# Performance work log

Hardware: AMD Instinct MI355X
Metric: run time of the kernel (lower is better)

The kernel has to match this reference:

```python
import jax, jax.numpy as jnp
import numpy as np

B, C, Ci, H, W = 4, 256, 128, 64, 64  # batch, in_channels, inter_channels, spatial
BN_EPS = 1e-5


def setup_inputs() -> dict:
    key = jax.random.key(0)
    ks = jax.random.split(key, 8)
    s = (2.0 / C) ** 0.5  # kaiming fan_in std for 1x1 conv over C inputs
    return {
        "a": jax.random.normal(ks[0], (B, C, H, W), jnp.float32),
        "b": jax.random.normal(ks[1], (B, C, H, W), jnp.float32),
        "theta_w": jax.random.normal(ks[2], (Ci, C), jnp.float32) * s,
        "theta_b": jnp.zeros((Ci,), jnp.float32),
        "phi_w": jax.random.normal(ks[3], (Ci, C), jnp.float32) * s,
        "phi_b": jnp.zeros((Ci,), jnp.float32),
        "g_w": jax.random.normal(ks[4], (Ci, C), jnp.float32) * s,
        "g_b": jnp.zeros((Ci,), jnp.float32),
        "W_w": jax.random.normal(ks[5], (C, Ci), jnp.float32) * (2.0 / Ci) ** 0.5,
        "bn_gamma": jnp.ones((C,), jnp.float32),
        "bn_beta": jnp.zeros((C,), jnp.float32),
        "bn_mean": jnp.zeros((C,), jnp.float32),
        "bn_var": jnp.ones((C,), jnp.float32),
    }


def _conv1x1(x, w, bias=None):
    # x: [B,Cin,H,W], w: [Cout,Cin] -> [B,Cout,H,W]
    y = jnp.einsum("oc,bchw->bohw", w, x)
    if bias is not None:
        y = y + bias[None, :, None, None]
    return y


def reference(a, b, theta_w, theta_b, phi_w, phi_b, g_w, g_b, W_w,
              bn_gamma, bn_beta, bn_mean, bn_var):
    Bsz, _, h, w = a.shape
    n = h * w
    theta_a = _conv1x1(a, theta_w, theta_b).reshape(Bsz, Ci, n).transpose(0, 2, 1)  # [B,N,Ci]
    phi_b_ = _conv1x1(b, phi_w, phi_b).reshape(Bsz, Ci, n)                          # [B,Ci,N]
    f = jnp.einsum("bnc,bcm->bnm", theta_a, phi_b_) / n                             # [B,N,N]
    g_b_ = _conv1x1(b, g_w, g_b).reshape(Bsz, Ci, n).transpose(0, 2, 1)             # [B,N,Ci]
    y = jnp.einsum("bnm,bmc->bnc", f, g_b_)                                         # [B,N,Ci]
    y = y.transpose(0, 2, 1).reshape(Bsz, Ci, h, w)
    wy = _conv1x1(y, W_w)                                                           # no bias
    inv = jax.lax.rsqrt(bn_var + BN_EPS)
    out = (wy - bn_mean[None, :, None, None]) * (bn_gamma * inv)[None, :, None, None] \
          + bn_beta[None, :, None, None]
    return out
```

## Files before the change

### kernel.cpp

```cpp
#include <hip/hip_runtime.h>
#include <hip/hip_bf16.h>

#define NSP 4096
#define CCH 256
#define CIN 128
#define BN_EPS 1e-5f

typedef __bf16 bf16x8 __attribute__((ext_vector_type(8)));
typedef __bf16 bf16x4 __attribute__((ext_vector_type(4)));
typedef float f32x4 __attribute__((ext_vector_type(4)));
typedef unsigned short u16x8 __attribute__((ext_vector_type(8)));

typedef const __attribute__((address_space(1))) unsigned int gu32;
typedef __attribute__((address_space(3))) unsigned int lu32;

__constant__ int IT10[10] = {0,0,0,0,1,1,1,2,2,3};
__constant__ int JT10[10] = {0,1,2,3,1,2,3,2,3,3};


__device__ __forceinline__ float4 fetch_tr(const float* __restrict__ A, int lda, int m0,
                                           int k0, int tid) {
  const int r = tid >> 2, kq = (tid & 3) << 2;
  return *(const float4*)(A + (size_t)(m0 + r) * lda + k0 + kq);
}
__device__ __forceinline__ void stash_tr(float (*As)[68], float4 v, int tid) {
  const int r = tid >> 2, kq = (tid & 3) << 2;
  As[kq + 0][r] = v.x; As[kq + 1][r] = v.y; As[kq + 2][r] = v.z; As[kq + 3][r] = v.w;
}
__device__ __forceinline__ float4 fetch_dir(const float* __restrict__ B, int ldb, int k0,
                                            int n0, int tid) {
  const int kr = tid >> 4, nq = (tid & 15) << 2;
  return *(const float4*)(B + (size_t)(k0 + kr) * ldb + n0 + nq);
}
__device__ __forceinline__ void stash_dir(float (*Bs)[68], float4 v, int tid) {
  const int kr = tid >> 4, nq = (tid & 15) << 2;
  *(float4*)(&Bs[kr][nq]) = v;
}

__device__ __forceinline__ void mm16(const float (*As)[68], const float (*Bs)[68],
                                     float acc[4][4], int ty, int tx) {
#pragma unroll
  for (int kk = 0; kk < 16; ++kk) {
    const float4 av = *(const float4*)(&As[kk][ty << 2]);
    const float4 bv = *(const float4*)(&Bs[kk][tx << 2]);
    const float ar[4] = {av.x, av.y, av.z, av.w};
    const float br[4] = {bv.x, bv.y, bv.z, bv.w};
#pragma unroll
    for (int i = 0; i < 4; ++i)
#pragma unroll
      for (int j = 0; j < 4; ++j) acc[i][j] += ar[i] * br[j];
  }
}

__device__ __forceinline__ float wave_reduce(float v) {
#pragma unroll
  for (int off = 32; off; off >>= 1) v += __shfl_down(v, off);
  return v;
}

__global__ __launch_bounds__(256) void prep_kernel(
    const float* __restrict__ bin, const float* __restrict__ a,
    const float* __restrict__ W_w, const float* __restrict__ g_w,
    const float* __restrict__ phi_w, const float* __restrict__ theta_w,
    const float* __restrict__ phi_b, const float* __restrict__ theta_b,
    const float* __restrict__ g_b,
    __bf16* __restrict__ bhi, __bf16* __restrict__ blo,
    float* __restrict__ srow,
    float* __restrict__ Wg, __bf16* __restrict__ Wghi, __bf16* __restrict__ Wglo,
    __bf16* __restrict__ PTthi, __bf16* __restrict__ PTtlo,
    __bf16* __restrict__ at,
    float* __restrict__ vb_g, float* __restrict__ vpt, float* __restrict__ wgb,
    float* __restrict__ dvec) {
  __shared__ float smem[64 * 68];
  const int idx = blockIdx.x;
  const int t = threadIdx.x;
  const int wave = t >> 6, lane = t & 63;
  if (idx < 1024) {
    const int row = idx;
    const float* src = bin + (size_t)row * NSP + t * 16;
    float sum = 0.f;
    unsigned short h16[16], l16[16];
#pragma unroll
    for (int i = 0; i < 4; ++i) {
      const float4 v = *(const float4*)(src + i * 4);
      const float vv[4] = {v.x, v.y, v.z, v.w};
      sum += v.x + v.y + v.z + v.w;
#pragma unroll
      for (int e = 0; e < 4; ++e) {
        const unsigned u = __float_as_uint(vv[e]);
        h16[i * 4 + e] = (unsigned short)(u >> 16);
        const float hf = __uint_as_float(u & 0xffff0000u);
        l16[i * 4 + e] = (unsigned short)(__float_as_uint(vv[e] - hf) >> 16);
      }
    }
    unsigned short* dh = (unsigned short*)bhi + (size_t)row * NSP + t * 16;
    unsigned short* dl = (unsigned short*)blo + (size_t)row * NSP + t * 16;
    *(u16x8*)dh = *(u16x8*)&h16[0];
    *(u16x8*)(dh + 8) = *(u16x8*)&h16[8];
    *(u16x8*)dl = *(u16x8*)&l16[0];
    *(u16x8*)(dl + 8) = *(u16x8*)&l16[8];
#pragma unroll
    for (int off = 32; off; off >>= 1) sum += __shfl_down(sum, off);
    if (lane == 0) smem[wave] = sum;
    __syncthreads();
    if (t == 0) srow[row] = smem[0] + smem[1] + smem[2] + smem[3];
  } else if (idx < 2048) {
    const int p = idx - 1024;
    const int n0 = (p & 63) * 64, c0 = ((p >> 6) & 3) * 64, b = p >> 8;
    float (*tile)[68] = (float(*)[68])smem;
    const int cr = t >> 4, nq = (t & 15) << 2;
    const float* src = a + ((size_t)(b * CCH + c0)) * NSP + n0;
#pragma unroll
    for (int s = 0; s < 4; ++s) {
      const float4 v = *(const float4*)(src + (size_t)(cr + s * 16) * NSP + nq);
      *(float4*)&tile[cr + s * 16][nq] = v;
    }
    __syncthreads();
    const int n = t >> 2, cq = (t & 3) << 4;
    __bf16 outv[16];
#pragma unroll
    for (int i = 0; i < 16; ++i) outv[i] = (__bf16)tile[cq + i][n];
    __bf16* dst = at + ((size_t)(b * NSP + n0 + n)) * CCH + c0 + cq;
    *(bf16x8*)dst = *(bf16x8*)&outv[0];
    *(bf16x8*)(dst + 8) = *(bf16x8*)&outv[8];
  } else if (idx < 2080) {
    const int p = idx - 2048;
    const int zsel = p >> 4, rem = p & 15;
    const int m0 = (rem >> 2) * 64, n0 = (rem & 3) * 64;
    float (*As)[68] = (float(*)[68])smem;
    float (*Bs)[68] = (float(*)[68])(smem + 16 * 68);
    const int ty = t >> 4, tx = t & 15;
    float acc[4][4] = {};
    if (zsel == 0) {
      float4 ar = fetch_tr(W_w, CIN, m0, 0, t);
      float4 br = fetch_dir(g_w, CCH, 0, n0, t);
      for (int kt = 0; kt < 8; ++kt) {
        stash_tr(As, ar, t); stash_dir(Bs, br, t);
        __syncthreads();
        if (kt < 7) { ar = fetch_tr(W_w, CIN, m0, (kt + 1) * 16, t);
                      br = fetch_dir(g_w, CCH, (kt + 1) * 16, n0, t); }
        mm16(As, Bs, acc, ty, tx);
        __syncthreads();
      }
#pragma unroll
      for (int i = 0; i < 4; ++i) {
        const size_t off = (size_t)(m0 + (ty << 2) + i) * 256 + n0 + (tx << 2);
        *(float4*)(Wg + off) = make_float4(acc[i][0], acc[i][1], acc[i][2], acc[i][3]);
        __bf16 h4[4], l4[4];
#pragma unroll
        for (int j = 0; j < 4; ++j) {
          const __bf16 h = (__bf16)acc[i][j];
          h4[j] = h; l4[j] = (__bf16)(acc[i][j] - (float)h);
        }
        *(bf16x4*)(Wghi + off) = *(bf16x4*)h4;
        *(bf16x4*)(Wglo + off) = *(bf16x4*)l4;
      }
    } else {
      float4 ar = fetch_dir(theta_w, CCH, 0, m0, t);
      float4 br = fetch_dir(phi_w, CCH, 0, n0, t);
      for (int kt = 0; kt < 8; ++kt) {
        stash_dir(As, ar, t); stash_dir(Bs, br, t);
        __syncthreads();
        if (kt < 7) { ar = fetch_dir(theta_w, CCH, (kt + 1) * 16, m0, t);
                      br = fetch_dir(phi_w, CCH, (kt + 1) * 16, n0, t); }
        mm16(As, Bs, acc, ty, tx);
        __syncthreads();
      }
#pragma unroll
      for (int i = 0; i < 4; ++i) {
        const size_t off = (size_t)(m0 + (ty << 2) + i) * 256 + n0 + (tx << 2);
        __bf16 h4[4], l4[4];
#pragma unroll
        for (int j = 0; j < 4; ++j) {
          const __bf16 h = (__bf16)acc[i][j];
          h4[j] = h; l4[j] = (__bf16)(acc[i][j] - (float)h);
        }
        *(bf16x4*)(PTthi + off) = *(bf16x4*)h4;
        *(bf16x4*)(PTtlo + off) = *(bf16x4*)l4;
      }
    }
  } else if (idx == 2080) {
    float* tb_s = smem;
    float* pb_s = smem + 128;
    if (t < 128) { tb_s[t] = theta_b[t]; pb_s[t] = phi_b[t]; }
    __syncthreads();
    float acc = 0.f;
#pragma unroll 8
    for (int i = 0; i < 128; ++i) acc += phi_w[(size_t)i * 256 + t] * tb_s[i];
    vb_g[t] = acc;
    if (t < 64) {
      float pv = pb_s[t] * tb_s[t] + pb_s[t + 64] * tb_s[t + 64];
      pv = wave_reduce(pv);
      if (t == 0) dvec[0] = pv;
    }
  } else if (idx == 2081) {
    float* pb_s = smem;
    if (t < 128) pb_s[t] = phi_b[t];
    __syncthreads();
    float acc = 0.f;
#pragma unroll 8
    for (int i = 0; i < 128; ++i) acc += pb_s[i] * theta_w[(size_t)i * 256 + t];
    vpt[t] = acc;
  } else {
    const int p = idx - 2082;
    float* gb_s = smem;
    if (t < 128) gb_s[t] = g_b[t];
    __syncthreads();
    const float2 gv = *(const float2*)&gb_s[lane * 2];
    for (int i = 0; i < 16; ++i) {
      const int o = p * 64 + wave * 16 + i;
      const float2 r = *(const float2*)(W_w + (size_t)o * 128 + lane * 2);
      float v = fmaf(r.x, gv.x, r.y * gv.y);
      v = wave_reduce(v);
      if (lane == 0) wgb[o] = v;
    }
  }
}

__global__ __launch_bounds__(256) void gram_kernel(
    const __bf16* __restrict__ bhi, const __bf16* __restrict__ blo,
    float* __restrict__ Gpart,
    const float* __restrict__ srow, const float* __restrict__ Wg,
    const __bf16* __restrict__ PTthi, const __bf16* __restrict__ PTtlo,
    const float* __restrict__ vb_g,
    float* __restrict__ Wgs, float* __restrict__ sPTv, float* __restrict__ dvec) {
  __shared__ __align__(16) __bf16 AtBt[2][2][64][64];
  auto& At = AtBt[0];
  auto& Bt = AtBt[1];
  const int idx = blockIdx.x;
  const int t = threadIdx.x;
  const int wave = t >> 6, lane = t & 63;
  if (idx < 320) {
    const int kc = idx & 7;
    const int rest = idx >> 3;
    const int tile = rest % 10;
    const int batch = rest / 10;
    const int it = IT10[tile], jt = JT10[tile];
    const bool diag = (it == jt);
    const int m = lane & 15, q = lane >> 4;
    const size_t rowbase = (size_t)batch * CCH;
    const int colbase = kc * 512;
    const int rseg = lane >> 3, ch = lane & 7;
    const int u = ch ^ rseg;
    const int h = u >> 2, j = u & 3;
    const __bf16* gsrc = h ? blo : bhi;

    auto stage = [&](int ph, int ks) {
#pragma unroll
      for (int c = 0; c < 4; ++c) {
        const int s = wave * 4 + c;
        const int isB = s >> 3;
        if (diag && isB) continue;
        const int kb = s & 7;
        const int grow = (isB ? jt : it) * 64 + kb * 8 + rseg;
        const __bf16* gp = gsrc + (rowbase + (size_t)grow) * NSP +
                           colbase + ks * 32 + j * 8;
        const __bf16* lp = isB ? &Bt[ph][kb * 8][0] : &At[ph][kb * 8][0];
        __builtin_amdgcn_global_load_lds((gu32*)(const void*)gp,
                                         (lu32*)(void*)lp, 16, 0, 0);
      }
    };

    f32x4 acc[4] = {};
    const int chA = q ^ (m & 7);
    stage(0, 0);
    int ph = 0;
    for (int ks = 0; ks < 16; ++ks) {
      __syncthreads();
      if (ks < 15) stage(ph ^ 1, ks + 1);
      const bf16x8 ah = *(const bf16x8*)&At[ph][wave * 16 + m][chA * 8];
      const bf16x8 al = *(const bf16x8*)&At[ph][wave * 16 + m][(chA ^ 4) * 8];
      const __bf16 (*Bsrc)[64] = diag ? At[ph] : Bt[ph];
#pragma unroll
      for (int t4 = 0; t4 < 4; ++t4) {
        const bf16x8 bh = *(const bf16x8*)&Bsrc[t4 * 16 + m][chA * 8];
        const bf16x8 bl = *(const bf16x8*)&Bsrc[t4 * 16 + m][(chA ^ 4) * 8];
        acc[t4] = __builtin_amdgcn_mfma_f32_16x16x32_bf16(ah, bh, acc[t4], 0, 0, 0);
        acc[t4] = __builtin_amdgcn_mfma_f32_16x16x32_bf16(ah, bl, acc[t4], 0, 0, 0);
        acc[t4] = __builtin_amdgcn_mfma_f32_16x16x32_bf16(al, bh, acc[t4], 0, 0, 0);
      }
      ph ^= 1;
    }
    float* Gp = Gpart + ((size_t)(kc * 4 + batch)) * 65536;
#pragma unroll
    for (int t4 = 0; t4 < 4; ++t4)
#pragma unroll
      for (int r = 0; r < 4; ++r)
        Gp[(size_t)(it * 64 + wave * 16 + q * 4 + r) * 256 + jt * 64 + t4 * 16 + m] =
            acc[t4][r];
    if (!diag) {
      __syncthreads();
      float* Tf = (float*)AtBt;
#pragma unroll
      for (int t4 = 0; t4 < 4; ++t4)
#pragma unroll
        for (int r = 0; r < 4; ++r)
          Tf[(t4 * 16 + m) * 68 + wave * 16 + q * 4 + r] = acc[t4][r];
      __syncthreads();
      const int rr = t >> 2, cq = (t & 3) * 16;
      float* Gpt = Gp + (size_t)(jt * 64 + rr) * 256 + it * 64 + cq;
#pragma unroll
      for (int i = 0; i < 4; ++i)
        *(float4*)(Gpt + i * 4) = *(const float4*)&Tf[rr * 68 + cq + i * 4];
    }
  } else {
    float* lds = (float*)AtBt;
    const int p = idx - 320;
    const int b = p >> 4, seg = p & 15;
    lds[t] = srow[b * 256 + t];
    __syncthreads();
    const float4 sv = *(const float4*)&lds[lane * 4];
    for (int i = wave; i < 16; i += 4) {
      const int o = seg * 16 + i;
      const float4 r = *(const float4*)(Wg + (size_t)o * 256 + lane * 4);
      float v = fmaf(r.x, sv.x, fmaf(r.y, sv.y, fmaf(r.z, sv.z, r.w * sv.w)));
      v = wave_reduce(v);
      if (lane == 0) Wgs[b * 256 + o] = v;
    }
    for (int i = wave; i < 16; i += 4) {
      const int c = seg * 16 + i;
      const bf16x4 ph = *(const bf16x4*)(PTthi + (size_t)c * 256 + lane * 4);
      const bf16x4 pl = *(const bf16x4*)(PTtlo + (size_t)c * 256 + lane * 4);
      const float svv[4] = {sv.x, sv.y, sv.z, sv.w};
      float v = 0.f;
#pragma unroll
      for (int e = 0; e < 4; ++e) v += ((float)ph[e] + (float)pl[e]) * svv[e];
      v = wave_reduce(v);
      if (lane == 0) sPTv[b * 256 + c] = v;
    }
    if (seg == 0 && wave == 0) {
      const float4 vbv = *(const float4*)(vb_g + lane * 4);
      float v = fmaf(vbv.x, sv.x, fmaf(vbv.y, sv.y, fmaf(vbv.z, sv.z, vbv.w * sv.w)));
      v = wave_reduce(v);
      if (lane == 0) dvec[1 + b] = v;
    }
  }
}

__global__ __launch_bounds__(256) void redw2_kernel(
    const float* __restrict__ Gpart, const float* __restrict__ vb_g,
    float* __restrict__ t2_g,
    const __bf16* __restrict__ Wghi, const __bf16* __restrict__ Wglo,
    __bf16* __restrict__ W2hi, __bf16* __restrict__ W2lo) {
  const int blk = blockIdx.x;
  const int t = threadIdx.x;
  const int wave = t >> 6, lane = t & 63;
  __shared__ __bf16 Gsh[16][264], Gsl[16][264];
  const int b = blk >> 4, nt = blk & 15;
  const int rr = t >> 4;
  const int c0 = (t & 15) * 16;
  f32x4 s[4] = {};
#pragma unroll
  for (int p = 0; p < 8; ++p) {
    const float* src = Gpart + (((size_t)(p * 4 + b)) << 16) +
                       (size_t)(nt * 16 + rr) * 256 + c0;
#pragma unroll
    for (int e = 0; e < 4; ++e) s[e] += *(const f32x4*)(src + e * 4);
  }
  {
    float part = 0.f;
#pragma unroll
    for (int e = 0; e < 4; ++e) {
      const float4 vv = *(const float4*)(vb_g + c0 + e * 4);
      part += s[e][0] * vv.x + s[e][1] * vv.y + s[e][2] * vv.z + s[e][3] * vv.w;
    }
#pragma unroll
    for (int off = 8; off; off >>= 1) part += __shfl_down(part, off);
    if ((t & 15) == 0) t2_g[b * 256 + nt * 16 + rr] = part;
  }
  __bf16 h8[16], l8[16];
#pragma unroll
  for (int e = 0; e < 16; ++e) {
    const float x = s[e >> 2][e & 3];
    const __bf16 h = (__bf16)x;
    h8[e] = h; l8[e] = (__bf16)(x - (float)h);
  }
  *(bf16x8*)&Gsh[rr][c0] = *(bf16x8*)&h8[0];
  *(bf16x8*)&Gsh[rr][c0 + 8] = *(bf16x8*)&h8[8];
  *(bf16x8*)&Gsl[rr][c0] = *(bf16x8*)&l8[0];
  *(bf16x8*)&Gsl[rr][c0 + 8] = *(bf16x8*)&l8[8];
  __syncthreads();
  const int m = lane & 15, q = lane >> 4;
  f32x4 acc[4] = {};
#pragma unroll
  for (int ks = 0; ks < 8; ++ks) {
    const int k = ks * 32 + q * 8;
    const bf16x8 bh = *(const bf16x8*)&Gsh[m][k];
    const bf16x8 bl = *(const bf16x8*)&Gsl[m][k];
#pragma unroll
    for (int i = 0; i < 4; ++i) {
      const int mt = i * 4 + wave;
      const bf16x8 ah = *(const bf16x8*)(Wghi + (size_t)(mt * 16 + m) * 256 + k);
      const bf16x8 al = *(const bf16x8*)(Wglo + (size_t)(mt * 16 + m) * 256 + k);
      acc[i] = __builtin_amdgcn_mfma_f32_16x16x32_bf16(ah, bh, acc[i], 0, 0, 0);
      acc[i] = __builtin_amdgcn_mfma_f32_16x16x32_bf16(ah, bl, acc[i], 0, 0, 0);
      acc[i] = __builtin_amdgcn_mfma_f32_16x16x32_bf16(al, bh, acc[i], 0, 0, 0);
    }
  }
#pragma unroll
  for (int i = 0; i < 4; ++i) {
    const int mt = i * 4 + wave;
#pragma unroll
    for (int r = 0; r < 4; ++r) {
      const size_t off = ((size_t)b << 16) + (size_t)(mt * 16 + q * 4 + r) * 256 +
                         nt * 16 + m;
      const float v = acc[i][r];
      const __bf16 h = (__bf16)v;
      W2hi[off] = h;
      W2lo[off] = (__bf16)(v - (float)h);
    }
  }
}

__global__ __launch_bounds__(256) void wout_mfma_kernel(
    const __bf16* __restrict__ W2hi, const __bf16* __restrict__ W2lo,
    const __bf16* __restrict__ PTthi, const __bf16* __restrict__ PTtlo,
    const float* __restrict__ Wgs, const float* __restrict__ sPT,
    const float* __restrict__ wgb, const float* __restrict__ vpt,
    const float* __restrict__ Wg, const float* __restrict__ t2_g,
    const float* __restrict__ dvec,
    const float* __restrict__ bn_gamma, const float* __restrict__ bn_beta,
    const float* __restrict__ bn_mean, const float* __restrict__ bn_var,
    __bf16* __restrict__ Whi, __bf16* __restrict__ Wlo,
    float* __restrict__ bias_out) {
  const int blk = blockIdx.x;
  const int t = threadIdx.x;
  const int wave = t >> 6, lane = t & 63;
  if (blk < 64) {
    const int batch = blk >> 4, nt = blk & 15;
    const int m = lane & 15, q = lane >> 4;
    const __bf16* bh_p = PTthi + (size_t)(nt * 16 + m) * 256;
    const __bf16* bl_p = PTtlo + (size_t)(nt * 16 + m) * 256;
    const __bf16* w2h = W2hi + (size_t)batch * 65536;
    const __bf16* w2l = W2lo + (size_t)batch * 65536;
    f32x4 acc[4] = {};
#pragma unroll
    for (int ks = 0; ks < 8; ++ks) {
      const int k = ks * 32 + q * 8;
      const bf16x8 bh = *(const bf16x8*)(bh_p + k);
      const bf16x8 bl = *(const bf16x8*)(bl_p + k);
#pragma unroll
      for (int i = 0; i < 4; ++i) {
        const int mt = i * 4 + wave;
        const bf16x8 ah = *(const bf16x8*)(w2h + (size_t)(mt * 16 + m) * 256 + k);
        const bf16x8 al = *(const bf16x8*)(w2l + (size_t)(mt * 16 + m) * 256 + k);
        acc[i] = __builtin_amdgcn_mfma_f32_16x16x32_bf16(ah, bh, acc[i], 0, 0, 0);
        acc[i] = __builtin_amdgcn_mfma_f32_16x16x32_bf16(ah, bl, acc[i], 0, 0, 0);
        acc[i] = __builtin_amdgcn_mfma_f32_16x16x32_bf16(al, bh, acc[i], 0, 0, 0);
      }
    }
    const float invN = 1.0f / 4096.0f;
    const int c = nt * 16 + m;
    const float vpt_c = vpt[c];
    const float sPT_c = sPT[batch * 256 + c];
#pragma unroll
    for (int i = 0; i < 4; ++i) {
      const int mt = i * 4 + wave;
#pragma unroll
      for (int r = 0; r < 4; ++r) {
        const int o = mt * 16 + q * 4 + r;
        const float sc = bn_gamma[o] * rsqrtf(bn_var[o] + BN_EPS);
        const float w = sc * ((acc[i][r] + Wgs[batch * 256 + o] * vpt_c + wgb[o] * sPT_c) * invN +
                              wgb[o] * vpt_c);
        const size_t off = (size_t)batch * 65536 + (size_t)o * 256 + c;
        const __bf16 h = (__bf16)w;
        Whi[off] = h;
        Wlo[off] = (__bf16)(w - (float)h);
      }
    }
  } else {
    const int p = blk - 64;
    const int b = p >> 2, quarter = p & 3;
    __shared__ float t2s[256];
    t2s[t] = t2_g[b * 256 + t];
    __syncthreads();
    const float d1 = dvec[0], d2 = dvec[1 + b];
    const float invN = 1.0f / 4096.0f;
    const float4 tv = *(const float4*)&t2s[lane * 4];
    for (int it = 0; it < 16; ++it) {
      const int o = quarter * 64 + wave * 16 + it;
      const float4 r = *(const float4*)(Wg + (size_t)o * 256 + lane * 4);
      float v = fmaf(r.x, tv.x, fmaf(r.y, tv.y, fmaf(r.z, tv.z, r.w * tv.w)));
      v = wave_reduce(v);
      if (lane == 0) {
        const float bias_full = (v + Wgs[b * 256 + o] * d1 +
                                 wgb[o] * (d2 + 4096.0f * d1)) * invN;
        const float sc = bn_gamma[o] * rsqrtf(bn_var[o] + BN_EPS);
        bias_out[b * 256 + o] = sc * (bias_full - bn_mean[o]) + bn_beta[o];
      }
    }
  }
}

__global__ __launch_bounds__(256) void out_mfma_kernel(const __bf16* __restrict__ Whi,
                                                       const __bf16* __restrict__ Wlo,
                                                       const __bf16* __restrict__ at,
                                                       const float* __restrict__ bias_out,
                                                       float* __restrict__ out) {
  const int ng = blockIdx.x, mt = blockIdx.y, b = blockIdx.z;
  const int wave = threadIdx.x >> 6, lane = threadIdx.x & 63;
  const int m = lane & 15, q = lane >> 4;
  const int o = mt * 64 + wave * 16 + m;
  const __bf16* wh = Whi + (size_t)b * 65536 + (size_t)o * 256;
  const __bf16* wl = Wlo + (size_t)b * 65536 + (size_t)o * 256;
  bf16x8 ah[8], al[8];
#pragma unroll
  for (int ks = 0; ks < 8; ++ks) {
    ah[ks] = *(const bf16x8*)(wh + ks * 32 + q * 8);
    al[ks] = *(const bf16x8*)(wl + ks * 32 + q * 8);
  }
  float bo[4];
#pragma unroll
  for (int r = 0; r < 4; ++r)
    bo[r] = bias_out[b * 256 + mt * 64 + wave * 16 + q * 4 + r];
  float* ob = out + (size_t)b * CCH * NSP;
#pragma unroll
  for (int nt4 = 0; nt4 < 2; ++nt4) {
    const __bf16* atb = at + ((size_t)b * NSP + ng * 128 + nt4 * 64) * CCH;
    f32x4 acc[4] = {};
#pragma unroll
    for (int ks = 0; ks < 8; ++ks) {
      const int k = ks * 32 + q * 8;
#pragma unroll
      for (int t4 = 0; t4 < 4; ++t4) {
        const bf16x8 bh = *(const bf16x8*)(atb + (size_t)(t4 * 16 + m) * 256 + k);
        acc[t4] = __builtin_amdgcn_mfma_f32_16x16x32_bf16(ah[ks], bh, acc[t4], 0, 0, 0);
        acc[t4] = __builtin_amdgcn_mfma_f32_16x16x32_bf16(al[ks], bh, acc[t4], 0, 0, 0);
      }
    }
#pragma unroll
    for (int r = 0; r < 4; ++r) {
      const int orow = mt * 64 + wave * 16 + q * 4 + r;
#pragma unroll
      for (int t4 = 0; t4 < 4; ++t4)
        ob[(size_t)orow * NSP + ng * 128 + nt4 * 64 + t4 * 16 + m] = acc[t4][r] + bo[r];
    }
  }
}

extern "C" void kernel_launch(void* const* d_in, const int* in_sizes, int n_in,
                              void* d_out, int out_size, void* d_ws, size_t ws_size,
                              hipStream_t stream) {
  (void)in_sizes; (void)n_in; (void)out_size; (void)ws_size;
  const float* a       = (const float*)d_in[0];
  const float* bI      = (const float*)d_in[1];
  const float* theta_w = (const float*)d_in[2];
  const float* theta_b = (const float*)d_in[3];
  const float* phi_w   = (const float*)d_in[4];
  const float* phi_b   = (const float*)d_in[5];
  const float* g_w     = (const float*)d_in[6];
  const float* g_b     = (const float*)d_in[7];
  const float* W_w     = (const float*)d_in[8];
  const float* bn_gamma= (const float*)d_in[9];
  const float* bn_beta = (const float*)d_in[10];
  const float* bn_mean = (const float*)d_in[11];
  const float* bn_var  = (const float*)d_in[12];
  float* out = (float*)d_out;
  float* ws  = (float*)d_ws;

  float* Gpart    = ws;
  float* srow     = ws + 4194304;
  float* Wg       = ws + 4195328;
  float* bias_out = ws + 4260864;
  float* Wgs      = ws + 4261888;
  float* sPTv     = ws + 4262912;
  float* wgb      = ws + 4263936;
  float* vpt      = ws + 4264192;
  float* vb_g     = ws + 4264448;
  float* t2_g     = ws + 4264704;
  float* dvec     = ws + 4265728;
  __bf16* at    = (__bf16*)(ws + 4265984);
  __bf16* Wghi  = (__bf16*)(ws + 6363136);
  __bf16* Wglo  = (__bf16*)(ws + 6395904);
  __bf16* PTthi = (__bf16*)(ws + 6428672);
  __bf16* PTtlo = (__bf16*)(ws + 6461440);
  __bf16* W2hi  = (__bf16*)(ws + 6494208);
  __bf16* W2lo  = (__bf16*)(ws + 6625280);
  __bf16* Whi   = (__bf16*)(ws + 6756352);
  __bf16* Wlo   = (__bf16*)(ws + 6887424);
  __bf16* bhi   = (__bf16*)(ws + 7018496);
  __bf16* blo   = (__bf16*)(ws + 9115648);

  prep_kernel<<<dim3(2086), dim3(256), 0, stream>>>(bI, a, W_w, g_w, phi_w, theta_w,
                                                    phi_b, theta_b, g_b,
                                                    bhi, blo, srow, Wg, Wghi, Wglo,
                                                    PTthi, PTtlo, at,
                                                    vb_g, vpt, wgb, dvec);
  gram_kernel<<<dim3(384), dim3(256), 0, stream>>>(bhi, blo, Gpart, srow, Wg,
                                                   PTthi, PTtlo, vb_g,
                                                   Wgs, sPTv, dvec);
  redw2_kernel<<<dim3(64), dim3(256), 0, stream>>>(Gpart, vb_g, t2_g,
                                                   Wghi, Wglo, W2hi, W2lo);
  wout_mfma_kernel<<<dim3(80), dim3(256), 0, stream>>>(W2hi, W2lo, PTthi, PTtlo,
                                                       Wgs, sPTv, wgb, vpt, Wg, t2_g,
                                                       dvec, bn_gamma, bn_beta, bn_mean,
                                                       bn_var, Whi, Wlo, bias_out);
  out_mfma_kernel<<<dim3(32, 4, 4), dim3(256), 0, stream>>>(Whi, Wlo, at, bias_out, out);
}
```

Measured before the change: 170.4 us.

## Rebalance kernel stages so independent prep work overlaps the Gram computation

Splits the former prep kernel so only the b-cast/row-sum runs first. The transpose of a, the weight-product GEMMs and the bias vectors now run as extra blocks inside the Gram kernel. The former gram tail blocks (Wgs/sPT/dvec) move into the redw2 launch. The aim is to fill idle compute units during the Gram phase and shorten the critical path of the first launch, at the cost of larger heterogeneous grids and more shared-memory aliasing.

```diff
diff --git a/kernel.cpp b/kernel.cpp
--- a/kernel.cpp
+++ b/kernel.cpp
@@ -58,175 +58,60 @@
   return v;
 }
 
-__global__ __launch_bounds__(256) void prep_kernel(
-    const float* __restrict__ bin, const float* __restrict__ a,
+__global__ __launch_bounds__(256) void castb_kernel(
+    const float* __restrict__ bin,
+    __bf16* __restrict__ bhi, __bf16* __restrict__ blo,
+    float* __restrict__ srow) {
+  __shared__ float smem[4];
+  const int t = threadIdx.x;
+  const int wave = t >> 6, lane = t & 63;
+  const int row = blockIdx.x;
+  const float* src = bin + (size_t)row * NSP + t * 16;
+  float sum = 0.f;
+  unsigned short h16[16], l16[16];
+#pragma unroll
+  for (int i = 0; i < 4; ++i) {
+    const float4 v = *(const float4*)(src + i * 4);
+    const float vv[4] = {v.x, v.y, v.z, v.w};
+    sum += v.x + v.y + v.z + v.w;
+#pragma unroll
+    for (int e = 0; e < 4; ++e) {
+      const unsigned u = __float_as_uint(vv[e]);
+      h16[i * 4 + e] = (unsigned short)(u >> 16);
+      const float hf = __uint_as_float(u & 0xffff0000u);
+      l16[i * 4 + e] = (unsigned short)(__float_as_uint(vv[e] - hf) >> 16);
+    }
+  }
+  unsigned short* dh = (unsigned short*)bhi + (size_t)row * NSP + t * 16;
+  unsigned short* dl = (unsigned short*)blo + (size_t)row * NSP + t * 16;
+  *(u16x8*)dh = *(u16x8*)&h16[0];
+  *(u16x8*)(dh + 8) = *(u16x8*)&h16[8];
+  *(u16x8*)dl = *(u16x8*)&l16[0];
+  *(u16x8*)(dl + 8) = *(u16x8*)&l16[8];
+#pragma unroll
+  for (int off = 32; off; off >>= 1) sum += __shfl_down(sum, off);
+  if (lane == 0) smem[wave] = sum;
+  __syncthreads();
+  if (t == 0) srow[row] = smem[0] + smem[1] + smem[2] + smem[3];
+}
+
+__global__ __launch_bounds__(256) void gram_plus_kernel(
+    const __bf16* __restrict__ bhi, const __bf16* __restrict__ blo,
+    float* __restrict__ Gpart,
+    const float* __restrict__ a,
     const float* __restrict__ W_w, const float* __restrict__ g_w,
     const float* __restrict__ phi_w, const float* __restrict__ theta_w,
     const float* __restrict__ phi_b, const float* __restrict__ theta_b,
     const float* __restrict__ g_b,
-    __bf16* __restrict__ bhi, __bf16* __restrict__ blo,
-    float* __restrict__ srow,
     float* __restrict__ Wg, __bf16* __restrict__ Wghi, __bf16* __restrict__ Wglo,
     __bf16* __restrict__ PTthi, __bf16* __restrict__ PTtlo,
     __bf16* __restrict__ at,
     float* __restrict__ vb_g, float* __restrict__ vpt, float* __restrict__ wgb,
     float* __restrict__ dvec) {
-  __shared__ float smem[64 * 68];
-  const int idx = blockIdx.x;
-  const int t = threadIdx.x;
-  const int wave = t >> 6, lane = t & 63;
-  if (idx < 1024) {
-    const int row = idx;
-    const float* src = bin + (size_t)row * NSP + t * 16;
-    float sum = 0.f;
-    unsigned short h16[16], l16[16];
-#pragma unroll
-    for (int i = 0; i < 4; ++i) {
-      const float4 v = *(const float4*)(src + i * 4);
-      const float vv[4] = {v.x, v.y, v.z, v.w};
-      sum += v.x + v.y + v.z + v.w;
-#pragma unroll
-      for (int e = 0; e < 4; ++e) {
-        const unsigned u = __float_as_uint(vv[e]);
-        h16[i * 4 + e] = (unsigned short)(u >> 16);
-        const float hf = __uint_as_float(u & 0xffff0000u);
-        l16[i * 4 + e] = (unsigned short)(__float_as_uint(vv[e] - hf) >> 16);
-      }
-    }
-    unsigned short* dh = (unsigned short*)bhi + (size_t)row * NSP + t * 16;
-    unsigned short* dl = (unsigned short*)blo + (size_t)row * NSP + t * 16;
-    *(u16x8*)dh = *(u16x8*)&h16[0];
-    *(u16x8*)(dh + 8) = *(u16x8*)&h16[8];
-    *(u16x8*)dl = *(u16x8*)&l16[0];
-    *(u16x8*)(dl + 8) = *(u16x8*)&l16[8];
-#pragma unroll
-    for (int off = 32; off; off >>= 1) sum += __shfl_down(sum, off);
-    if (lane == 0) smem[wave] = sum;
-    __syncthreads();
-    if (t == 0) srow[row] = smem[0] + smem[1] + smem[2] + smem[3];
-  } else if (idx < 2048) {
-    const int p = idx - 1024;
-    const int n0 = (p & 63) * 64, c0 = ((p >> 6) & 3) * 64, b = p >> 8;
-    float (*tile)[68] = (float(*)[68])smem;
-    const int cr = t >> 4, nq = (t & 15) << 2;
-    const float* src = a + ((size_t)(b * CCH + c0)) * NSP + n0;
-#pragma unroll
-    for (int s = 0; s < 4; ++s) {
-      const float4 v = *(const float4*)(src + (size_t)(cr + s * 16) * NSP + nq);
-      *(float4*)&tile[cr + s * 16][nq] = v;
-    }
-    __syncthreads();
-    const int n = t >> 2, cq = (t & 3) << 4;
-    __bf16 outv[16];
-#pragma unroll
-    for (int i = 0; i < 16; ++i) outv[i] = (__bf16)tile[cq + i][n];
-    __bf16* dst = at + ((size_t)(b * NSP + n0 + n)) * CCH + c0 + cq;
-    *(bf16x8*)dst = *(bf16x8*)&outv[0];
-    *(bf16x8*)(dst + 8) = *(bf16x8*)&outv[8];
-  } else if (idx < 2080) {
-    const int p = idx - 2048;
-    const int zsel = p >> 4, rem = p & 15;
-    const int m0 = (rem >> 2) * 64, n0 = (rem & 3) * 64;
-    float (*As)[68] = (float(*)[68])smem;
-    float (*Bs)[68] = (float(*)[68])(smem + 16 * 68);
-    const int ty = t >> 4, tx = t & 15;
-    float acc[4][4] = {};
-    if (zsel == 0) {
-      float4 ar = fetch_tr(W_w, CIN, m0, 0, t);
-      float4 br = fetch_dir(g_w, CCH, 0, n0, t);
-      for (int kt = 0; kt < 8; ++kt) {
-        stash_tr(As, ar, t); stash_dir(Bs, br, t);
-        __syncthreads();
-        if (kt < 7) { ar = fetch_tr(W_w, CIN, m0, (kt + 1) * 16, t);
-                      br = fetch_dir(g_w, CCH, (kt + 1) * 16, n0, t); }
-        mm16(As, Bs, acc, ty, tx);
-        __syncthreads();
-      }
-#pragma unroll
-      for (int i = 0; i < 4; ++i) {
-        const size_t off = (size_t)(m0 + (ty << 2) + i) * 256 + n0 + (tx << 2);
-        *(float4*)(Wg + off) = make_float4(acc[i][0], acc[i][1], acc[i][2], acc[i][3]);
-        __bf16 h4[4], l4[4];
-#pragma unroll
-        for (int j = 0; j < 4; ++j) {
-          const __bf16 h = (__bf16)acc[i][j];
-          h4[j] = h; l4[j] = (__bf16)(acc[i][j] - (float)h);
-        }
-        *(bf16x4*)(Wghi + off) = *(bf16x4*)h4;
-        *(bf16x4*)(Wglo + off) = *(bf16x4*)l4;
-      }
-    } else {
-      float4 ar = fetch_dir(theta_w, CCH, 0, m0, t);
-      float4 br = fetch_dir(phi_w, CCH, 0, n0, t);
-      for (int kt = 0; kt < 8; ++kt) {
-        stash_dir(As, ar, t); stash_dir(Bs, br, t);
-        __syncthreads();
-        if (kt < 7) { ar = fetch_dir(theta_w, CCH, (kt + 1) * 16, m0, t);
-                      br = fetch_dir(phi_w, CCH, (kt + 1) * 16, n0, t); }
-        mm16(As, Bs, acc, ty, tx);
-        __syncthreads();
-      }
-#pragma unroll
-      for (int i = 0; i < 4; ++i) {
-        const size_t off = (size_t)(m0 + (ty << 2) + i) * 256 + n0 + (tx << 2);
-        __bf16 h4[4], l4[4];
-#pragma unroll
-        for (int j = 0; j < 4; ++j) {
-          const __bf16 h = (__bf16)acc[i][j];
-          h4[j] = h; l4[j] = (__bf16)(acc[i][j] - (float)h);
-        }
-        *(bf16x4*)(PTthi + off) = *(bf16x4*)h4;
-        *(bf16x4*)(PTtlo + off) = *(bf16x4*)l4;
-      }
-    }
-  } else if (idx == 2080) {
-    float* tb_s = smem;
-    float* pb_s = smem + 128;
-    if (t < 128) { tb_s[t] = theta_b[t]; pb_s[t] = phi_b[t]; }
-    __syncthreads();
-    float acc = 0.f;
-#pragma unroll 8
-    for (int i = 0; i < 128; ++i) acc += phi_w[(size_t)i * 256 + t] * tb_s[i];
-    vb_g[t] = acc;
-    if (t < 64) {
-      float pv = pb_s[t] * tb_s[t] + pb_s[t + 64] * tb_s[t + 64];
-      pv = wave_reduce(pv);
-      if (t == 0) dvec[0] = pv;
-    }
-  } else if (idx == 2081) {
-    float* pb_s = smem;
-    if (t < 128) pb_s[t] = phi_b[t];
-    __syncthreads();
-    float acc = 0.f;
-#pragma unroll 8
-    for (int i = 0; i < 128; ++i) acc += pb_s[i] * theta_w[(size_t)i * 256 + t];
-    vpt[t] = acc;
-  } else {
-    const int p = idx - 2082;
-    float* gb_s = smem;
-    if (t < 128) gb_s[t] = g_b[t];
-    __syncthreads();
-    const float2 gv = *(const float2*)&gb_s[lane * 2];
-    for (int i = 0; i < 16; ++i) {
-      const int o = p * 64 + wave * 16 + i;
-      const float2 r = *(const float2*)(W_w + (size_t)o * 128 + lane * 2);
-      float v = fmaf(r.x, gv.x, r.y * gv.y);
-      v = wave_reduce(v);
-      if (lane == 0) wgb[o] = v;
-    }
-  }
-}
-
-__global__ __launch_bounds__(256) void gram_kernel(
-    const __bf16* __restrict__ bhi, const __bf16* __restrict__ blo,
-    float* __restrict__ Gpart,
-    const float* __restrict__ srow, const float* __restrict__ Wg,
-    const __bf16* __restrict__ PTthi, const __bf16* __restrict__ PTtlo,
-    const float* __restrict__ vb_g,
-    float* __restrict__ Wgs, float* __restrict__ sPTv, float* __restrict__ dvec) {
   __shared__ __align__(16) __bf16 AtBt[2][2][64][64];
   auto& At = AtBt[0];
   auto& Bt = AtBt[1];
+  float* smem = (float*)AtBt;
   const int idx = blockIdx.x;
   const int t = threadIdx.x;
   const int wave = t >> 6, lane = t & 63;
@@ -303,9 +188,199 @@
       for (int i = 0; i < 4; ++i)
         *(float4*)(Gpt + i * 4) = *(const float4*)&Tf[rr * 68 + cq + i * 4];
     }
+  } else if (idx < 1344) {
+    const int p = idx - 320;
+    const int n0 = (p & 63) * 64, c0 = ((p >> 6) & 3) * 64, b = p >> 8;
+    float (*tile)[68] = (float(*)[68])smem;
+    const int cr = t >> 4, nq = (t & 15) << 2;
+    const float* src = a + ((size_t)(b * CCH + c0)) * NSP + n0;
+#pragma unroll
+    for (int s = 0; s < 4; ++s) {
+      const float4 v = *(const float4*)(src + (size_t)(cr + s * 16) * NSP + nq);
+      *(float4*)&tile[cr + s * 16][nq] = v;
+    }
+    __syncthreads();
+    const int n = t >> 2, cq = (t & 3) << 4;
+    __bf16 outv[16];
+#pragma unroll
+    for (int i = 0; i < 16; ++i) outv[i] = (__bf16)tile[cq + i][n];
+    __bf16* dst = at + ((size_t)(b * NSP + n0 + n)) * CCH + c0 + cq;
+    *(bf16x8*)dst = *(bf16x8*)&outv[0];
+    *(bf16x8*)(dst + 8) = *(bf16x8*)&outv[8];
+  } else if (idx < 1376) {
+    const int p = idx - 1344;
+    const int zsel = p >> 4, rem = p & 15;
+    const int m0 = (rem >> 2) * 64, n0 = (rem & 3) * 64;
+    float (*As)[68] = (float(*)[68])smem;
+    float (*Bs)[68] = (float(*)[68])(smem + 16 * 68);
+    const int ty = t >> 4, tx = t & 15;
+    float acc[4][4] = {};
+    if (zsel == 0) {
+      float4 ar = fetch_tr(W_w, CIN, m0, 0, t);
+      float4 br = fetch_dir(g_w, CCH, 0, n0, t);
+      for (int kt = 0; kt < 8; ++kt) {
+        stash_tr(As, ar, t); stash_dir(Bs, br, t);
+        __syncthreads();
+        if (kt < 7) { ar = fetch_tr(W_w, CIN, m0, (kt + 1) * 16, t);
+                      br = fetch_dir(g_w, CCH, (kt + 1) * 16, n0, t); }
+        mm16(As, Bs, acc, ty, tx);
+        __syncthreads();
+      }
+#pragma unroll
+      for (int i = 0; i < 4; ++i) {
+        const size_t off = (size_t)(m0 + (ty << 2) + i) * 256 + n0 + (tx << 2);
+        *(float4*)(Wg + off) = make_float4(acc[i][0], acc[i][1], acc[i][2], acc[i][3]);
+        __bf16 h4[4], l4[4];
+#pragma unroll
+        for (int j = 0; j < 4; ++j) {
+          const __bf16 h = (__bf16)acc[i][j];
+          h4[j] = h; l4[j] = (__bf16)(acc[i][j] - (float)h);
+        }
+        *(bf16x4*)(Wghi + off) = *(bf16x4*)h4;
+        *(bf16x4*)(Wglo + off) = *(bf16x4*)l4;
+      }
+    } else {
+      float4 ar = fetch_dir(theta_w, CCH, 0, m0, t);
+      float4 br = fetch_dir(phi_w, CCH, 0, n0, t);
+      for (int kt = 0; kt < 8; ++kt) {
+        stash_dir(As, ar, t); stash_dir(Bs, br, t);
+        __syncthreads();
+        if (kt < 7) { ar = fetch_dir(theta_w, CCH, (kt + 1) * 16, m0, t);
+                      br = fetch_dir(phi_w, CCH, (kt + 1) * 16, n0, t); }
+        mm16(As, Bs, acc, ty, tx);
+        __syncthreads();
+      }
+#pragma unroll
+      for (int i = 0; i < 4; ++i) {
+        const size_t off = (size_t)(m0 + (ty << 2) + i) * 256 + n0 + (tx << 2);
+        __bf16 h4[4], l4[4];
+#pragma unroll
+        for (int j = 0; j < 4; ++j) {
+          const __bf16 h = (__bf16)acc[i][j];
+          h4[j] = h; l4[j] = (__bf16)(acc[i][j] - (float)h);
+        }
+        *(bf16x4*)(PTthi + off) = *(bf16x4*)h4;
+        *(bf16x4*)(PTtlo + off) = *(bf16x4*)l4;
+      }
+    }
+  } else if (idx == 1376) {
+    float* tb_s = smem;
+    float* pb_s = smem + 128;
+    if (t < 128) { tb_s[t] = theta_b[t]; pb_s[t] = phi_b[t]; }
+    __syncthreads();
+    float acc = 0.f;
+#pragma unroll 8
+    for (int i = 0; i < 128; ++i) acc += phi_w[(size_t)i * 256 + t] * tb_s[i];
+    vb_g[t] = acc;
+    if (t < 64) {
+      float pv = pb_s[t] * tb_s[t] + pb_s[t + 64] * tb_s[t + 64];
+      pv = wave_reduce(pv);
+      if (t == 0) dvec[0] = pv;
+    }
+  } else if (idx == 1377) {
+    float* pb_s = smem;
+    if (t < 128) pb_s[t] = phi_b[t];
+    __syncthreads();
+    float acc = 0.f;
+#pragma unroll 8
+    for (int i = 0; i < 128; ++i) acc += pb_s[i] * theta_w[(size_t)i * 256 + t];
+    vpt[t] = acc;
   } else {
-    float* lds = (float*)AtBt;
-    const int p = idx - 320;
+    const int p = idx - 1378;
+    float* gb_s = smem;
+    if (t < 128) gb_s[t] = g_b[t];
+    __syncthreads();
+    const float2 gv = *(const float2*)&gb_s[lane * 2];
+    for (int i = 0; i < 16; ++i) {
+      const int o = p * 64 + wave * 16 + i;
+      const float2 r = *(const float2*)(W_w + (size_t)o * 128 + lane * 2);
+      float v = fmaf(r.x, gv.x, r.y * gv.y);
+      v = wave_reduce(v);
+      if (lane == 0) wgb[o] = v;
+    }
+  }
+}
+
+__global__ __launch_bounds__(256) void redw2_kernel(
+    const float* __restrict__ Gpart, const float* __restrict__ vb_g,
+    float* __restrict__ t2_g, const float* __restrict__ srow,
+    const float* __restrict__ Wg,
+    const __bf16* __restrict__ Wghi, const __bf16* __restrict__ Wglo,
+    const __bf16* __restrict__ PTthi, const __bf16* __restrict__ PTtlo,
+    __bf16* __restrict__ W2hi, __bf16* __restrict__ W2lo,
+    float* __restrict__ Wgs, float* __restrict__ sPTv, float* __restrict__ dvec) {
+  const int blk = blockIdx.x;
+  const int t = threadIdx.x;
+  const int wave = t >> 6, lane = t & 63;
+  __shared__ __bf16 Gsh[16][264], Gsl[16][264];
+  __shared__ float lds[256];
+  if (blk < 64) {
+    const int b = blk >> 4, nt = blk & 15;
+    const int rr = t >> 4;
+    const int c0 = (t & 15) * 16;
+    f32x4 s[4] = {};
+#pragma unroll
+    for (int p = 0; p < 8; ++p) {
+      const float* src = Gpart + (((size_t)(p * 4 + b)) << 16) +
+                         (size_t)(nt * 16 + rr) * 256 + c0;
+#pragma unroll
+      for (int e = 0; e < 4; ++e) s[e] += *(const f32x4*)(src + e * 4);
+    }
+    {
+      float part = 0.f;
+#pragma unroll
+      for (int e = 0; e < 4; ++e) {
+        const float4 vv = *(const float4*)(vb_g + c0 + e * 4);
+        part += s[e][0] * vv.x + s[e][1] * vv.y + s[e][2] * vv.z + s[e][3] * vv.w;
+      }
+#pragma unroll
+      for (int off = 8; off; off >>= 1) part += __shfl_down(part, off);
+      if ((t & 15) == 0) t2_g[b * 256 + nt * 16 + rr] = part;
+    }
+    __bf16 h8[16], l8[16];
+#pragma unroll
+    for (int e = 0; e < 16; ++e) {
+      const float x = s[e >> 2][e & 3];
+      const __bf16 h = (__bf16)x;
+      h8[e] = h; l8[e] = (__bf16)(x - (float)h);
+    }
+    *(bf16x8*)&Gsh[rr][c0] = *(bf16x8*)&h8[0];
+    *(bf16x8*)&Gsh[rr][c0 + 8] = *(bf16x8*)&h8[8];
+    *(bf16x8*)&Gsl[rr][c0] = *(bf16x8*)&l8[0];
+    *(bf16x8*)&Gsl[rr][c0 + 8] = *(bf16x8*)&l8[8];
+    __syncthreads();
+    const int m = lane & 15, q = lane >> 4;
+    f32x4 acc[4] = {};
+#pragma unroll
+    for (int ks = 0; ks < 8; ++ks) {
+      const int k = ks * 32 + q * 8;
+      const bf16x8 bh = *(const bf16x8*)&Gsh[m][k];
+      const bf16x8 bl = *(const bf16x8*)&Gsl[m][k];
+#pragma unroll
+      for (int i = 0; i < 4; ++i) {
+        const int mt = i * 4 + wave;
+        const bf16x8 ah = *(const bf16x8*)(Wghi + (size_t)(mt * 16 + m) * 256 + k);
+        const bf16x8 al = *(const bf16x8*)(Wglo + (size_t)(mt * 16 + m) * 256 + k);
+        acc[i] = __builtin_amdgcn_mfma_f32_16x16x32_bf16(ah, bh, acc[i], 0, 0, 0);
+        acc[i] = __builtin_amdgcn_mfma_f32_16x16x32_bf16(ah, bl, acc[i], 0, 0, 0);
+        acc[i] = __builtin_amdgcn_mfma_f32_16x16x32_bf16(al, bh, acc[i], 0, 0, 0);
+      }
+    }
+#pragma unroll
+    for (int i = 0; i < 4; ++i) {
+      const int mt = i * 4 + wave;
+#pragma unroll
+      for (int r = 0; r < 4; ++r) {
+        const size_t off = ((size_t)b << 16) + (size_t)(mt * 16 + q * 4 + r) * 256 +
+                           nt * 16 + m;
+        const float v = acc[i][r];
+        const __bf16 h = (__bf16)v;
+        W2hi[off] = h;
+        W2lo[off] = (__bf16)(v - (float)h);
+      }
+    }
+  } else {
+    const int p = blk - 64;
     const int b = p >> 4, seg = p & 15;
     lds[t] = srow[b * 256 + t];
     __syncthreads();
@@ -333,81 +408,6 @@
       float v = fmaf(vbv.x, sv.x, fmaf(vbv.y, sv.y, fmaf(vbv.z, sv.z, vbv.w * sv.w)));
       v = wave_reduce(v);
       if (lane == 0) dvec[1 + b] = v;
-    }
-  }
-}
-
-__global__ __launch_bounds__(256) void redw2_kernel(
-    const float* __restrict__ Gpart, const float* __restrict__ vb_g,
-    float* __restrict__ t2_g,
-    const __bf16* __restrict__ Wghi, const __bf16* __restrict__ Wglo,
-    __bf16* __restrict__ W2hi, __bf16* __restrict__ W2lo) {
-  const int blk = blockIdx.x;
-  const int t = threadIdx.x;
-  const int wave = t >> 6, lane = t & 63;
-  __shared__ __bf16 Gsh[16][264], Gsl[16][264];
-  const int b = blk >> 4, nt = blk & 15;
-  const int rr = t >> 4;
-  const int c0 = (t & 15) * 16;
-  f32x4 s[4] = {};
-#pragma unroll
-  for (int p = 0; p < 8; ++p) {
-    const float* src = Gpart + (((size_t)(p * 4 + b)) << 16) +
-                       (size_t)(nt * 16 + rr) * 256 + c0;
-#pragma unroll
-    for (int e = 0; e < 4; ++e) s[e] += *(const f32x4*)(src + e * 4);
-  }
-  {
-    float part = 0.f;
-#pragma unroll
-    for (int e = 0; e < 4; ++e) {
-      const float4 vv = *(const float4*)(vb_g + c0 + e * 4);
-      part += s[e][0] * vv.x + s[e][1] * vv.y + s[e][2] * vv.z + s[e][3] * vv.w;
-    }
-#pragma unroll
-    for (int off = 8; off; off >>= 1) part += __shfl_down(part, off);
-    if ((t & 15) == 0) t2_g[b * 256 + nt * 16 + rr] = part;
-  }
-  __bf16 h8[16], l8[16];
-#pragma unroll
-  for (int e = 0; e < 16; ++e) {
-    const float x = s[e >> 2][e & 3];
-    const __bf16 h = (__bf16)x;
-    h8[e] = h; l8[e] = (__bf16)(x - (float)h);
-  }
-  *(bf16x8*)&Gsh[rr][c0] = *(bf16x8*)&h8[0];
-  *(bf16x8*)&Gsh[rr][c0 + 8] = *(bf16x8*)&h8[8];
-  *(bf16x8*)&Gsl[rr][c0] = *(bf16x8*)&l8[0];
-  *(bf16x8*)&Gsl[rr][c0 + 8] = *(bf16x8*)&l8[8];
-  __syncthreads();
-  const int m = lane & 15, q = lane >> 4;
-  f32x4 acc[4] = {};
-#pragma unroll
-  for (int ks = 0; ks < 8; ++ks) {
-    const int k = ks * 32 + q * 8;
-    const bf16x8 bh = *(const bf16x8*)&Gsh[m][k];
-    const bf16x8 bl = *(const bf16x8*)&Gsl[m][k];
-#pragma unroll
-    for (int i = 0; i < 4; ++i) {
-      const int mt = i * 4 + wave;
-      const bf16x8 ah = *(const bf16x8*)(Wghi + (size_t)(mt * 16 + m) * 256 + k);
-      const bf16x8 al = *(const bf16x8*)(Wglo + (size_t)(mt * 16 + m) * 256 + k);
-      acc[i] = __builtin_amdgcn_mfma_f32_16x16x32_bf16(ah, bh, acc[i], 0, 0, 0);
-      acc[i] = __builtin_amdgcn_mfma_f32_16x16x32_bf16(ah, bl, acc[i], 0, 0, 0);
-      acc[i] = __builtin_amdgcn_mfma_f32_16x16x32_bf16(al, bh, acc[i], 0, 0, 0);
-    }
-  }
-#pragma unroll
-  for (int i = 0; i < 4; ++i) {
-    const int mt = i * 4 + wave;
-#pragma unroll
-    for (int r = 0; r < 4; ++r) {
-      const size_t off = ((size_t)b << 16) + (size_t)(mt * 16 + q * 4 + r) * 256 +
-                         nt * 16 + m;
-      const float v = acc[i][r];
-      const __bf16 h = (__bf16)v;
-      W2hi[off] = h;
-      W2lo[off] = (__bf16)(v - (float)h);
     }
   }
 }
@@ -581,16 +581,15 @@
   __bf16* bhi   = (__bf16*)(ws + 7018496);
   __bf16* blo   = (__bf16*)(ws + 9115648);
 
-  prep_kernel<<<dim3(2086), dim3(256), 0, stream>>>(bI, a, W_w, g_w, phi_w, theta_w,
-                                                    phi_b, theta_b, g_b,
-                                                    bhi, blo, srow, Wg, Wghi, Wglo,
-                                                    PTthi, PTtlo, at,
-                                                    vb_g, vpt, wgb, dvec);
-  gram_kernel<<<dim3(384), dim3(256), 0, stream>>>(bhi, blo, Gpart, srow, Wg,
-                                                   PTthi, PTtlo, vb_g,
-                                                   Wgs, sPTv, dvec);
-  redw2_kernel<<<dim3(64), dim3(256), 0, stream>>>(Gpart, vb_g, t2_g,
-                                                   Wghi, Wglo, W2hi, W2lo);
+  castb_kernel<<<dim3(1024), dim3(256), 0, stream>>>(bI, bhi, blo, srow);
+  gram_plus_kernel<<<dim3(1382), dim3(256), 0, stream>>>(bhi, blo, Gpart, a,
+                                                         W_w, g_w, phi_w, theta_w,
+                                                         phi_b, theta_b, g_b,
+                                                         Wg, Wghi, Wglo, PTthi, PTtlo,
+                                                         at, vb_g, vpt, wgb, dvec);
+  redw2_kernel<<<dim3(128), dim3(256), 0, stream>>>(Gpart, vb_g, t2_g, srow, Wg,
+                                                    Wghi, Wglo, PTthi, PTtlo,
+                                                    W2hi, W2lo, Wgs, sPTv, dvec);
   wout_mfma_kernel<<<dim3(80), dim3(256), 0, stream>>>(W2hi, W2lo, PTthi, PTtlo,
                                                        Wgs, sPTv, wgb, vpt, Wg, t2_g,
                                                        dvec, bn_gamma, bn_beta, bn_mean,
```

After: 165.1 us. -3.1%, faster.
